# Kernel optimization log

Hardware: AMD Instinct MI355X
Metric: run time of the kernel (lower is better)

## Reference

```python
import jax, jax.numpy as jnp
import numpy as np

N = 4_000_000   # number of (parent, child) edges
N_RELS = 20
P = 3            # n_polarities
Z_EPS = 0.01
COS_EPS = 0.01
SCALE_FACTOR = 42.0


def setup_inputs() -> dict:
    key = jax.random.key(0)
    k1, k2, k3, k4, k5, k6, k7 = jax.random.split(key, 7)
    child_probs = jax.random.uniform(k1, (N, P), dtype=jnp.float32)
    prnt_probs = jax.random.uniform(k2, (N, P), dtype=jnp.float32)
    child_probs = child_probs * (jax.random.uniform(k3, (N, 1)) > 0.1).astype(jnp.float32)
    prnt_probs = prnt_probs * (jax.random.uniform(k4, (N, 1)) > 0.1).astype(jnp.float32)
    rels = jax.random.randint(k5, (N,), 0, N_RELS)
    eps_M = jax.random.normal(k6, (N, P, P), dtype=jnp.float32)
    beta = jax.random.beta(k7, 15.0, 15.0, (N,), dtype=jnp.float32)  # Beta(beta_p, beta_q), all 15.0
    # learned/fixed params per __init__
    MU = np.eye(P, dtype=np.float32)
    MU[1, :] = [-0.25, 0.5, -0.25]
    rel_mu = jnp.asarray(np.tile(MU, (N_RELS, 1)).reshape(N_RELS, P, P))
    rel_sigma = jnp.ones((N_RELS, P, P), dtype=jnp.float32)
    return {"prnt_probs": prnt_probs, "child_probs": child_probs, "rel_mu": rel_mu,
            "rel_sigma": rel_sigma, "eps_M": eps_M, "beta": beta, "rels": rels}


def _safe_norm(x):
    sq = jnp.sum(x * x, axis=-1)
    return jnp.where(sq == 0.0, 0.0, jnp.sqrt(jnp.where(sq == 0.0, 1.0, sq)))


def _scale(prnt, child):
    # z = max(eps, p + c); normalize; entropy; cosine similarity; scale = 42 * cos / H(z)
    z = jnp.maximum(Z_EPS, prnt + child)
    z = z / jnp.sum(z, axis=-1, keepdims=True)
    entropy = -jnp.sum(z * jnp.log(z), axis=-1)
    cos = jnp.sum(prnt * child, axis=-1)
    norm = _safe_norm(prnt) * _safe_norm(child)
    norm = jnp.where(norm == 0.0, 1.0, norm)
    cos = jnp.maximum(COS_EPS, cos / norm)
    return SCALE_FACTOR * cos / entropy


def reference(prnt_probs, child_probs, rel_mu, rel_sigma, eps_M, beta, rels):
    # mask-based equivalent of the nonzero()-gather version (static shapes for jit)
    child_mask = jnp.sum(child_probs, axis=-1) != 0.0          # rows with nonzero child probs
    # M ~ Normal(mu[rels], sigma[rels]) reparameterized
    M = rel_mu[rels] + rel_sigma[rels] * eps_M                  # [N, P, P]
    cp = jax.nn.softmax(jnp.einsum('nij,nj->ni', M, child_probs), axis=-1)  # [N, P]
    prnt_sum = jnp.sum(prnt_probs, axis=-1)
    copy_mask = child_mask & (prnt_sum == 0.0)                  # child copied to parent
    alpha_mask = child_mask & (prnt_sum != 0.0)                 # blended update
    s = _scale(prnt_probs, cp)                                  # [N]
    alpha = ((1.0 - beta)[:, None] * prnt_probs + beta[:, None] * cp) * s[:, None]
    child_probs2copy = jnp.where(copy_mask[:, None], cp, 0.0)
    alpha = jnp.where(alpha_mask[:, None], alpha, 0.0)
    return copy_mask, child_probs2copy, alpha_mask, alpha
```

## Files before the change

### kernel.cpp

```cpp
#include <hip/hip_runtime.h>

#define BLOCK 256

__global__ __launch_bounds__(BLOCK) void alpha_kernel(
    const float4* __restrict__ prnt4,
    const float4* __restrict__ child4,
    const float*  __restrict__ rel_mu,
    const float*  __restrict__ rel_sigma,
    const float4* __restrict__ eps4,
    const float4* __restrict__ beta4,
    const int4*   __restrict__ rels4,
    float4* __restrict__ out0,
    float4* __restrict__ out1,
    float4* __restrict__ out2,
    float4* __restrict__ out3,
    int ngroups, int nmu)
{
    __shared__ float smu[192];
    __shared__ float ssg[192];
    for (int i = threadIdx.x; i < nmu; i += BLOCK) {
        smu[i] = rel_mu[i];
        ssg[i] = rel_sigma[i];
    }
    __syncthreads();

    int t = blockIdx.x * BLOCK + threadIdx.x;
    if (t >= ngroups) return;

    float p[12], c[12], e[36];
    {
        float4 v;
        #pragma unroll
        for (int k = 0; k < 3; ++k) {
            v = prnt4[3 * t + k];
            p[4*k+0] = v.x; p[4*k+1] = v.y; p[4*k+2] = v.z; p[4*k+3] = v.w;
        }
        #pragma unroll
        for (int k = 0; k < 3; ++k) {
            v = child4[3 * t + k];
            c[4*k+0] = v.x; c[4*k+1] = v.y; c[4*k+2] = v.z; c[4*k+3] = v.w;
        }
        #pragma unroll
        for (int k = 0; k < 9; ++k) {
            v = eps4[9 * t + k];
            e[4*k+0] = v.x; e[4*k+1] = v.y; e[4*k+2] = v.z; e[4*k+3] = v.w;
        }
    }
    float4 btv = beta4[t];
    int4   rv  = rels4[t];
    float bq[4] = {btv.x, btv.y, btv.z, btv.w};
    int   rq[4] = {rv.x, rv.y, rv.z, rv.w};

    float o0[4], o2[4], o1[12], o3[12];

    #pragma unroll
    for (int q = 0; q < 4; ++q) {
        const float* pp = &p[3 * q];
        const float* cc = &c[3 * q];
        const float* ee = &e[9 * q];
        const float* mu = &smu[9 * rq[q]];
        const float* sg = &ssg[9 * rq[q]];

        float l[3];
        #pragma unroll
        for (int i = 0; i < 3; ++i) {
            float acc = 0.0f;
            #pragma unroll
            for (int j = 0; j < 3; ++j) {
                float m = fmaf(sg[3*i+j], ee[3*i+j], mu[3*i+j]);
                acc = fmaf(m, cc[j], acc);
            }
            l[i] = acc;
        }
        float mx = fmaxf(l[0], fmaxf(l[1], l[2]));
        float e0 = __expf(l[0] - mx), e1 = __expf(l[1] - mx), e2 = __expf(l[2] - mx);
        float einv = 1.0f / (e0 + e1 + e2);
        float cp0 = e0 * einv, cp1 = e1 * einv, cp2 = e2 * einv;

        float csum = cc[0] + cc[1] + cc[2];
        float psum = pp[0] + pp[1] + pp[2];
        bool cmask = (csum != 0.0f);
        bool copy  = cmask && (psum == 0.0f);
        bool amask = cmask && (psum != 0.0f);

        float z0 = fmaxf(0.01f, pp[0] + cp0);
        float z1 = fmaxf(0.01f, pp[1] + cp1);
        float z2 = fmaxf(0.01f, pp[2] + cp2);
        float zinv = 1.0f / (z0 + z1 + z2);
        z0 *= zinv; z1 *= zinv; z2 *= zinv;
        float ent = -(z0 * __logf(z0) + z1 * __logf(z1) + z2 * __logf(z2));
        float cosv = pp[0]*cp0 + pp[1]*cp1 + pp[2]*cp2;
        float np2 = pp[0]*pp[0] + pp[1]*pp[1] + pp[2]*pp[2];
        float nc2 = cp0*cp0 + cp1*cp1 + cp2*cp2;
        float npn = (np2 == 0.0f) ? 0.0f : sqrtf(np2);
        float ncn = (nc2 == 0.0f) ? 0.0f : sqrtf(nc2);
        float nrm = npn * ncn;
        nrm = (nrm == 0.0f) ? 1.0f : nrm;
        cosv = fmaxf(0.01f, cosv / nrm);
        float s = 42.0f * cosv / ent;

        float b = bq[q], ob = 1.0f - b;
        float a0 = fmaf(ob, pp[0], b * cp0) * s;
        float a1 = fmaf(ob, pp[1], b * cp1) * s;
        float a2 = fmaf(ob, pp[2], b * cp2) * s;

        o0[q] = copy  ? 1.0f : 0.0f;
        o2[q] = amask ? 1.0f : 0.0f;
        o1[3*q+0] = copy ? cp0 : 0.0f;
        o1[3*q+1] = copy ? cp1 : 0.0f;
        o1[3*q+2] = copy ? cp2 : 0.0f;
        o3[3*q+0] = amask ? a0 : 0.0f;
        o3[3*q+1] = amask ? a1 : 0.0f;
        o3[3*q+2] = amask ? a2 : 0.0f;
    }

    out0[t] = make_float4(o0[0], o0[1], o0[2], o0[3]);
    out2[t] = make_float4(o2[0], o2[1], o2[2], o2[3]);
    #pragma unroll
    for (int k = 0; k < 3; ++k) {
        out1[3*t+k] = make_float4(o1[4*k+0], o1[4*k+1], o1[4*k+2], o1[4*k+3]);
        out3[3*t+k] = make_float4(o3[4*k+0], o3[4*k+1], o3[4*k+2], o3[4*k+3]);
    }
}

extern "C" void kernel_launch(void* const* d_in, const int* in_sizes, int n_in,
                              void* d_out, int out_size, void* d_ws, size_t ws_size,
                              hipStream_t stream)
{
    const float* prnt      = (const float*)d_in[0];
    const float* child     = (const float*)d_in[1];
    const float* rel_mu    = (const float*)d_in[2];
    const float* rel_sigma = (const float*)d_in[3];
    const float* eps       = (const float*)d_in[4];
    const float* beta      = (const float*)d_in[5];
    const int*   rels      = (const int*)d_in[6];

    const int N = in_sizes[5];
    const int ngroups = N / 4;
    const int nmu = in_sizes[2];

    float* out  = (float*)d_out;
    float* out0 = out;
    float* out1 = out + (size_t)N;
    float* out2 = out + (size_t)4 * N;
    float* out3 = out + (size_t)5 * N;

    int blocks = (ngroups + BLOCK - 1) / BLOCK;
    alpha_kernel<<<blocks, BLOCK, 0, stream>>>(
        (const float4*)prnt, (const float4*)child, rel_mu, rel_sigma,
        (const float4*)eps, (const float4*)beta, (const int4*)rels,
        (float4*)out0, (float4*)out1, (float4*)out2, (float4*)out3,
        ngroups, nmu);
}
```

Measured before the change: 355.1 us.

## Stage row data through shared memory for coalesced loads and stores

Each block now cooperatively loads 512 rows of parent, child and eps data into LDS with fully coalesced float4 accesses. Each thread then processes 2 rows from shared memory, and the 3-wide outputs are staged back through LDS before a coalesced write-out. Before this, every thread loaded strided float4 chunks of 48 to 144 bytes, which left global accesses poorly coalesced. The cost is extra LDS traffic, two more barriers, about 27KB of shared memory per block (which may limit occupancy), and possible LDS bank conflicts from the stride-6 and stride-18 reads.

```diff
diff --git a/kernel.cpp b/kernel.cpp
--- a/kernel.cpp
+++ b/kernel.cpp
@@ -1,6 +1,9 @@
 #include <hip/hip_runtime.h>
 
 #define BLOCK 256
+#define ROWS  512
+#define PCF4  (ROWS * 3 / 4)
+#define EPSF4 (ROWS * 9 / 4)
 
 __global__ __launch_bounds__(BLOCK) void alpha_kernel(
     const float4* __restrict__ prnt4,
@@ -8,118 +11,153 @@
     const float*  __restrict__ rel_mu,
     const float*  __restrict__ rel_sigma,
     const float4* __restrict__ eps4,
-    const float4* __restrict__ beta4,
-    const int4*   __restrict__ rels4,
-    float4* __restrict__ out0,
+    const float2* __restrict__ beta2,
+    const int2*   __restrict__ rels2,
+    float2* __restrict__ out0,
     float4* __restrict__ out1,
-    float4* __restrict__ out2,
+    float2* __restrict__ out2,
     float4* __restrict__ out3,
-    int ngroups, int nmu)
+    int n_rows, int nmu)
 {
-    __shared__ float smu[192];
-    __shared__ float ssg[192];
+    __shared__ float4 s_p[PCF4];
+    __shared__ float4 s_c[PCF4];
+    __shared__ float4 s_e[EPSF4];
+    __shared__ float  smu[192];
+    __shared__ float  ssg[192];
+
     for (int i = threadIdx.x; i < nmu; i += BLOCK) {
         smu[i] = rel_mu[i];
         ssg[i] = rel_sigma[i];
     }
+
+    const int  b         = blockIdx.x;
+    const long rows_base = (long)b * ROWS;
+    const int  rows_here = min(ROWS, (int)(n_rows - rows_base));
+    const int  pcf4_here  = rows_here * 3 / 4;
+    const int  epsf4_here = rows_here * 9 / 4;
+
+    const float4* gp = prnt4  + (size_t)b * PCF4;
+    const float4* gc = child4 + (size_t)b * PCF4;
+    const float4* ge = eps4   + (size_t)b * EPSF4;
+
+    for (int i = threadIdx.x; i < pcf4_here; i += BLOCK) {
+        s_p[i] = gp[i];
+        s_c[i] = gc[i];
+    }
+    for (int i = threadIdx.x; i < epsf4_here; i += BLOCK) {
+        s_e[i] = ge[i];
+    }
     __syncthreads();
 
-    int t = blockIdx.x * BLOCK + threadIdx.x;
-    if (t >= ngroups) return;
+    const int  lt     = threadIdx.x;
+    const bool active = (lt < rows_here / 2);
 
-    float p[12], c[12], e[36];
-    {
-        float4 v;
+    float o1[6], o3[6];
+    float2 m0, m2;
+
+    if (active) {
+        const float* pf = (const float*)s_p;
+        const float* cf = (const float*)s_c;
+        const float* ef = (const float*)s_e;
+
+        float p[6], c[6], e[18];
         #pragma unroll
-        for (int k = 0; k < 3; ++k) {
-            v = prnt4[3 * t + k];
-            p[4*k+0] = v.x; p[4*k+1] = v.y; p[4*k+2] = v.z; p[4*k+3] = v.w;
+        for (int k = 0; k < 6; ++k)  p[k] = pf[6 * lt + k];
+        #pragma unroll
+        for (int k = 0; k < 6; ++k)  c[k] = cf[6 * lt + k];
+        #pragma unroll
+        for (int k = 0; k < 18; ++k) e[k] = ef[18 * lt + k];
+
+        float2 bt = beta2[rows_base / 2 + lt];
+        int2   rl = rels2[rows_base / 2 + lt];
+        float bq[2] = {bt.x, bt.y};
+        int   rq[2] = {rl.x, rl.y};
+
+        float mo0[2], mo2[2];
+
+        #pragma unroll
+        for (int q = 0; q < 2; ++q) {
+            const float* pp = &p[3 * q];
+            const float* cc = &c[3 * q];
+            const float* ee = &e[9 * q];
+            const float* mu = &smu[9 * rq[q]];
+            const float* sg = &ssg[9 * rq[q]];
+
+            float l[3];
+            #pragma unroll
+            for (int i = 0; i < 3; ++i) {
+                float acc = 0.0f;
+                #pragma unroll
+                for (int j = 0; j < 3; ++j) {
+                    float m = fmaf(sg[3 * i + j], ee[3 * i + j], mu[3 * i + j]);
+                    acc = fmaf(m, cc[j], acc);
+                }
+                l[i] = acc;
+            }
+            float mx = fmaxf(l[0], fmaxf(l[1], l[2]));
+            float e0 = __expf(l[0] - mx), e1 = __expf(l[1] - mx), e2 = __expf(l[2] - mx);
+            float einv = 1.0f / (e0 + e1 + e2);
+            float cp0 = e0 * einv, cp1 = e1 * einv, cp2 = e2 * einv;
+
+            float csum = cc[0] + cc[1] + cc[2];
+            float psum = pp[0] + pp[1] + pp[2];
+            bool cmask = (csum != 0.0f);
+            bool copy  = cmask && (psum == 0.0f);
+            bool amask = cmask && (psum != 0.0f);
+
+            float z0 = fmaxf(0.01f, pp[0] + cp0);
+            float z1 = fmaxf(0.01f, pp[1] + cp1);
+            float z2 = fmaxf(0.01f, pp[2] + cp2);
+            float zinv = 1.0f / (z0 + z1 + z2);
+            z0 *= zinv; z1 *= zinv; z2 *= zinv;
+            float ent = -(z0 * __logf(z0) + z1 * __logf(z1) + z2 * __logf(z2));
+            float cosv = pp[0] * cp0 + pp[1] * cp1 + pp[2] * cp2;
+            float np2 = pp[0] * pp[0] + pp[1] * pp[1] + pp[2] * pp[2];
+            float nc2 = cp0 * cp0 + cp1 * cp1 + cp2 * cp2;
+            float npn = (np2 == 0.0f) ? 0.0f : sqrtf(np2);
+            float ncn = (nc2 == 0.0f) ? 0.0f : sqrtf(nc2);
+            float nrm = npn * ncn;
+            nrm = (nrm == 0.0f) ? 1.0f : nrm;
+            cosv = fmaxf(0.01f, cosv / nrm);
+            float s = 42.0f * cosv / ent;
+
+            float bb = bq[q], ob = 1.0f - bb;
+            float a0 = fmaf(ob, pp[0], bb * cp0) * s;
+            float a1 = fmaf(ob, pp[1], bb * cp1) * s;
+            float a2 = fmaf(ob, pp[2], bb * cp2) * s;
+
+            mo0[q] = copy  ? 1.0f : 0.0f;
+            mo2[q] = amask ? 1.0f : 0.0f;
+            o1[3 * q + 0] = copy ? cp0 : 0.0f;
+            o1[3 * q + 1] = copy ? cp1 : 0.0f;
+            o1[3 * q + 2] = copy ? cp2 : 0.0f;
+            o3[3 * q + 0] = amask ? a0 : 0.0f;
+            o3[3 * q + 1] = amask ? a1 : 0.0f;
+            o3[3 * q + 2] = amask ? a2 : 0.0f;
         }
-        #pragma unroll
-        for (int k = 0; k < 3; ++k) {
-            v = child4[3 * t + k];
-            c[4*k+0] = v.x; c[4*k+1] = v.y; c[4*k+2] = v.z; c[4*k+3] = v.w;
-        }
-        #pragma unroll
-        for (int k = 0; k < 9; ++k) {
-            v = eps4[9 * t + k];
-            e[4*k+0] = v.x; e[4*k+1] = v.y; e[4*k+2] = v.z; e[4*k+3] = v.w;
-        }
-    }
-    float4 btv = beta4[t];
-    int4   rv  = rels4[t];
-    float bq[4] = {btv.x, btv.y, btv.z, btv.w};
-    int   rq[4] = {rv.x, rv.y, rv.z, rv.w};
-
-    float o0[4], o2[4], o1[12], o3[12];
-
-    #pragma unroll
-    for (int q = 0; q < 4; ++q) {
-        const float* pp = &p[3 * q];
-        const float* cc = &c[3 * q];
-        const float* ee = &e[9 * q];
-        const float* mu = &smu[9 * rq[q]];
-        const float* sg = &ssg[9 * rq[q]];
-
-        float l[3];
-        #pragma unroll
-        for (int i = 0; i < 3; ++i) {
-            float acc = 0.0f;
-            #pragma unroll
-            for (int j = 0; j < 3; ++j) {
-                float m = fmaf(sg[3*i+j], ee[3*i+j], mu[3*i+j]);
-                acc = fmaf(m, cc[j], acc);
-            }
-            l[i] = acc;
-        }
-        float mx = fmaxf(l[0], fmaxf(l[1], l[2]));
-        float e0 = __expf(l[0] - mx), e1 = __expf(l[1] - mx), e2 = __expf(l[2] - mx);
-        float einv = 1.0f / (e0 + e1 + e2);
-        float cp0 = e0 * einv, cp1 = e1 * einv, cp2 = e2 * einv;
-
-        float csum = cc[0] + cc[1] + cc[2];
-        float psum = pp[0] + pp[1] + pp[2];
-        bool cmask = (csum != 0.0f);
-        bool copy  = cmask && (psum == 0.0f);
-        bool amask = cmask && (psum != 0.0f);
-
-        float z0 = fmaxf(0.01f, pp[0] + cp0);
-        float z1 = fmaxf(0.01f, pp[1] + cp1);
-        float z2 = fmaxf(0.01f, pp[2] + cp2);
-        float zinv = 1.0f / (z0 + z1 + z2);
-        z0 *= zinv; z1 *= zinv; z2 *= zinv;
-        float ent = -(z0 * __logf(z0) + z1 * __logf(z1) + z2 * __logf(z2));
-        float cosv = pp[0]*cp0 + pp[1]*cp1 + pp[2]*cp2;
-        float np2 = pp[0]*pp[0] + pp[1]*pp[1] + pp[2]*pp[2];
-        float nc2 = cp0*cp0 + cp1*cp1 + cp2*cp2;
-        float npn = (np2 == 0.0f) ? 0.0f : sqrtf(np2);
-        float ncn = (nc2 == 0.0f) ? 0.0f : sqrtf(nc2);
-        float nrm = npn * ncn;
-        nrm = (nrm == 0.0f) ? 1.0f : nrm;
-        cosv = fmaxf(0.01f, cosv / nrm);
-        float s = 42.0f * cosv / ent;
-
-        float b = bq[q], ob = 1.0f - b;
-        float a0 = fmaf(ob, pp[0], b * cp0) * s;
-        float a1 = fmaf(ob, pp[1], b * cp1) * s;
-        float a2 = fmaf(ob, pp[2], b * cp2) * s;
-
-        o0[q] = copy  ? 1.0f : 0.0f;
-        o2[q] = amask ? 1.0f : 0.0f;
-        o1[3*q+0] = copy ? cp0 : 0.0f;
-        o1[3*q+1] = copy ? cp1 : 0.0f;
-        o1[3*q+2] = copy ? cp2 : 0.0f;
-        o3[3*q+0] = amask ? a0 : 0.0f;
-        o3[3*q+1] = amask ? a1 : 0.0f;
-        o3[3*q+2] = amask ? a2 : 0.0f;
+        m0 = make_float2(mo0[0], mo0[1]);
+        m2 = make_float2(mo2[0], mo2[1]);
     }
 
-    out0[t] = make_float4(o0[0], o0[1], o0[2], o0[3]);
-    out2[t] = make_float4(o2[0], o2[1], o2[2], o2[3]);
-    #pragma unroll
-    for (int k = 0; k < 3; ++k) {
-        out1[3*t+k] = make_float4(o1[4*k+0], o1[4*k+1], o1[4*k+2], o1[4*k+3]);
-        out3[3*t+k] = make_float4(o3[4*k+0], o3[4*k+1], o3[4*k+2], o3[4*k+3]);
+    __syncthreads();
+
+    if (active) {
+        float* of1 = (float*)s_p;
+        float* of3 = (float*)s_c;
+        #pragma unroll
+        for (int k = 0; k < 6; ++k) of1[6 * lt + k] = o1[k];
+        #pragma unroll
+        for (int k = 0; k < 6; ++k) of3[6 * lt + k] = o3[k];
+        out0[rows_base / 2 + lt] = m0;
+        out2[rows_base / 2 + lt] = m2;
+    }
+    __syncthreads();
+
+    float4* g1 = out1 + (size_t)b * PCF4;
+    float4* g3 = out3 + (size_t)b * PCF4;
+    for (int i = threadIdx.x; i < pcf4_here; i += BLOCK) {
+        g1[i] = s_p[i];
+        g3[i] = s_c[i];
     }
 }
 
@@ -135,8 +173,7 @@
     const float* beta      = (const float*)d_in[5];
     const int*   rels      = (const int*)d_in[6];
 
-    const int N = in_sizes[5];
-    const int ngroups = N / 4;
+    const int N   = in_sizes[5];
     const int nmu = in_sizes[2];
 
     float* out  = (float*)d_out;
@@ -145,10 +182,10 @@
     float* out2 = out + (size_t)4 * N;
     float* out3 = out + (size_t)5 * N;
 
-    int blocks = (ngroups + BLOCK - 1) / BLOCK;
+    int blocks = (N + ROWS - 1) / ROWS;
     alpha_kernel<<<blocks, BLOCK, 0, stream>>>(
         (const float4*)prnt, (const float4*)child, rel_mu, rel_sigma,
-        (const float4*)eps, (const float4*)beta, (const int4*)rels,
-        (float4*)out0, (float4*)out1, (float4*)out2, (float4*)out3,
-        ngroups, nmu);
+        (const float4*)eps, (const float2*)beta, (const int2*)rels,
+        (float2*)out0, (float4*)out1, (float2*)out2, (float4*)out3,
+        N, nmu);
 }
```

Measured after the change: 335.3 us. -5.6%, faster.
